# Performance work log

Measured on AMD Instinct MI355X. Metric: run time of the kernel, lower is better.

The kernel has to match this reference:

```python
import jax, jax.numpy as jnp
import numpy as np

IN_C, OUT_C, K, N_FILTERS, STRIDE, PAD = 256, 512, 3, 64, 1, 1


def setup_inputs() -> dict:
    key = jax.random.key(0)
    kx, kw, kb, krw, krb = jax.random.split(key, 5)
    fan_in = IN_C * K * K
    bound = 1.0 / np.sqrt(fan_in)
    x = jax.random.normal(kx, (32, IN_C, 56, 56), dtype=jnp.float32)
    weight = jax.random.uniform(kw, (OUT_C, IN_C, K, K), minval=-bound, maxval=bound, dtype=jnp.float32)
    bias = jax.random.uniform(kb, (OUT_C,), minval=-bound, maxval=bound, dtype=jnp.float32)
    rbound = 1.0 / np.sqrt(IN_C)
    router_w = jax.random.uniform(krw, (OUT_C, IN_C), minval=-rbound, maxval=rbound, dtype=jnp.float32)
    router_b = jax.random.uniform(krb, (OUT_C,), minval=-rbound, maxval=rbound, dtype=jnp.float32)
    return {"x": x, "weight": weight, "bias": bias, "router_w": router_w, "router_b": router_b}


def reference(x, weight, bias, router_w, router_b):
    B = x.shape[0]
    # router: global avg pool -> linear -> top-k channel mask
    pooled = jnp.mean(x, axis=(2, 3))                      # [B, IN_C]
    router_out = pooled @ router_w.T + router_b            # [B, OUT_C]
    _, top_idx = jax.lax.top_k(router_out, N_FILTERS)      # [B, k]
    mask = jnp.zeros((B, OUT_C), dtype=x.dtype).at[jnp.arange(B)[:, None], top_idx].set(1.0)
    # dense conv2d
    conv = jax.lax.conv_general_dilated(
        x, weight, window_strides=(STRIDE, STRIDE), padding=[(PAD, PAD), (PAD, PAD)],
        dimension_numbers=("NCHW", "OIHW", "NCHW"))
    conv = conv + bias[None, :, None, None]
    return conv * mask[:, :, None, None]
```

## Files before the change

### kernel.cpp

```cpp
#include <hip/hip_runtime.h>

#define IN_C   256
#define OUT_C  512
#define WIDTH  56
#define HW     3136
#define KTOT   2304
#define NF     64
#define NU     448
#define NB     32
#define NGRP   8
#define TN     64
#define NTILE  49
#define XROWS  178
#define LDX    40

typedef __bf16 bf16x8 __attribute__((ext_vector_type(8)));
typedef float  f32x4  __attribute__((ext_vector_type(4)));

__global__ __launch_bounds__(256) void pool_kernel(const float* __restrict__ x,
                                                   float* __restrict__ pooled) {
    int bc = blockIdx.x;
    const float4* src = (const float4*)(x + (size_t)bc * HW);
    float s = 0.f;
    for (int i = threadIdx.x; i < HW / 4; i += 256) {
        float4 v = src[i];
        s += v.x + v.y + v.z + v.w;
    }
    #pragma unroll
    for (int off = 32; off > 0; off >>= 1) s += __shfl_down(s, off, 64);
    __shared__ float wsum[4];
    int lane = threadIdx.x & 63, wv = threadIdx.x >> 6;
    if (lane == 0) wsum[wv] = s;
    __syncthreads();
    if (threadIdx.x == 0)
        pooled[bc] = (wsum[0] + wsum[1] + wsum[2] + wsum[3]) * (1.0f / HW);
}

__global__ __launch_bounds__(512) void router_kernel(const float* __restrict__ pooled,
                                                     const float* __restrict__ rw,
                                                     const float* __restrict__ rb,
                                                     int* __restrict__ sel,
                                                     int* __restrict__ unsel) {
    int b = blockIdx.x;
    __shared__ float p[IN_C];
    __shared__ float v[OUT_C];
    __shared__ int   scount, ucount;
    int t = threadIdx.x;
    if (t < IN_C) p[t] = pooled[b * IN_C + t];
    if (t == 0) { scount = 0; ucount = 0; }
    __syncthreads();
    float acc = rb[t];
    const float* wrow = rw + (size_t)t * IN_C;
    for (int i = 0; i < IN_C; ++i) acc += p[i] * wrow[i];
    v[t] = acc;
    __syncthreads();
    int cnt = 0;
    for (int j = 0; j < OUT_C; ++j) {
        float o = v[j];
        cnt += (o > acc) || (o == acc && j < t);
    }
    if (cnt < NF) {
        int pos = atomicAdd(&scount, 1);
        sel[b * NF + pos] = t;
    } else {
        int pos = atomicAdd(&ucount, 1);
        unsel[b * NU + pos] = t;
    }
}

__global__ __launch_bounds__(256) void compact_w(const float* __restrict__ w,
                                                 const int* __restrict__ sel,
                                                 __bf16* __restrict__ Acomp) {
    int id = blockIdx.x;
    int b = id / 72, rem = id - b * 72;
    int g = rem / 9, tap = rem - g * 9;
    int t = threadIdx.x;
    int oc = t >> 2, q = t & 3;
    int s = sel[b * NF + oc];
    const float* wsrc = w + (size_t)s * KTOT + tap;
    bf16x8 o;
    #pragma unroll
    for (int j = 0; j < 8; ++j)
        o[j] = (__bf16)wsrc[(g * 32 + q * 8 + j) * 9];
    *(bf16x8*)&Acomp[((size_t)id * 64 + oc) * 32 + q * 8] = o;
}

__global__ __launch_bounds__(64) void conv_kernel(const float* __restrict__ x,
                                                  const __bf16* __restrict__ Acomp,
                                                  const float* __restrict__ bias,
                                                  const int* __restrict__ sel,
                                                  const int* __restrict__ unsel,
                                                  float* __restrict__ out) {
    int id   = blockIdx.x;
    int xcd  = id & 7, slot = id >> 3;
    int bq   = slot / NTILE;
    int tile = slot - bq * NTILE;
    int b    = xcd * 4 + bq;
    int ptile = tile * TN;

    int lane = threadIdx.x;
    int fm   = lane & 15, fq = lane >> 4;

    __shared__ __bf16 xlds[XROWS * LDX];

    size_t outb = (size_t)b * OUT_C * HW;

    {
        const int* unselb = unsel + b * NU;
        f32x4 z = {0.f, 0.f, 0.f, 0.f};
        for (int u = fq; u < NU; u += 4) {
            int oc = unselb[u];
            __builtin_nontemporal_store(z, (f32x4*)(out + outb + (size_t)oc * HW + ptile) + fm);
        }
    }

    const float*  x_b    = x + (size_t)b * IN_C * HW;
    const __bf16* a_base = Acomp + (size_t)b * (NGRP * 9 * 64 * 32);

    int pp[4], poh[4], pow_[4];
    #pragma unroll
    for (int s = 0; s < 4; ++s) {
        int p = ptile + s * 16 + fm;
        pp[s]   = p;
        poh[s]  = p / WIDTH;
        pow_[s] = p - poh[s] * WIDTH;
    }

    int gp0[3]; bool act[3];
    #pragma unroll
    for (int it = 0; it < 3; ++it) {
        int sp = it * 64 + lane;
        act[it] = sp < XROWS;
        int gp = ptile - 57 + sp;
        gp = gp < 0 ? 0 : (gp > HW - 1 ? HW - 1 : gp);
        gp0[it] = gp;
    }

    f32x4 acc[4][4] = {};

    #pragma unroll 1
    for (int g = 0; g < NGRP; ++g) {
        #pragma unroll
        for (int it = 0; it < 3; ++it) {
            if (!act[it]) continue;
            int sp = it * 64 + lane;
            const float* sx = x_b + (size_t)(g * 32) * HW + gp0[it];
            #pragma unroll
            for (int oct = 0; oct < 4; ++oct) {
                float v[8];
                #pragma unroll
                for (int j = 0; j < 8; ++j) v[j] = sx[(size_t)(oct * 8 + j) * HW];
                bf16x8 o;
                #pragma unroll
                for (int j = 0; j < 8; ++j) o[j] = (__bf16)v[j];
                *(bf16x8*)&xlds[sp * LDX + oct * 8] = o;
            }
        }
        const __bf16* gp_a = a_base + (size_t)g * 9 * 64 * 32;
        #pragma unroll
        for (int t9 = 0; t9 < 9; ++t9) {
            const int r = t9 / 3, c = t9 - 3 * (t9 / 3);
            const int shift = (r - 1) * WIDTH + (c - 1);
            const __bf16* ap = gp_a + (size_t)t9 * 64 * 32;
            bf16x8 af[4];
            #pragma unroll
            for (int mi = 0; mi < 4; ++mi)
                af[mi] = *(const bf16x8*)(ap + (size_t)(mi * 16 + fm) * 32 + fq * 8);
            #pragma unroll
            for (int s = 0; s < 4; ++s) {
                int ohr = poh[s] + r - 1, owc = pow_[s] + c - 1;
                bool ok = ((unsigned)ohr < 56u) && ((unsigned)owc < 56u);
                bf16x8 bfr = *(const bf16x8*)&xlds[(s * 16 + fm + 57 + shift) * LDX + fq * 8];
                bf16x8 zz = {};
                bfr = ok ? bfr : zz;
                #pragma unroll
                for (int mi = 0; mi < 4; ++mi)
                    acc[mi][s] = __builtin_amdgcn_mfma_f32_16x16x32_bf16(af[mi], bfr, acc[mi][s], 0, 0, 0);
            }
        }
    }

    const int* selb = sel + b * NF;
    #pragma unroll
    for (int mi = 0; mi < 4; ++mi) {
        #pragma unroll
        for (int reg = 0; reg < 4; ++reg) {
            int oc = selb[mi * 16 + fq * 4 + reg];
            float bs = bias[oc];
            float* orow = out + outb + (size_t)oc * HW;
            #pragma unroll
            for (int s = 0; s < 4; ++s)
                __builtin_nontemporal_store(acc[mi][s][reg] + bs, &orow[pp[s]]);
        }
    }
}

extern "C" void kernel_launch(void* const* d_in, const int* in_sizes, int n_in,
                              void* d_out, int out_size, void* d_ws, size_t ws_size,
                              hipStream_t stream) {
    (void)in_sizes; (void)n_in; (void)ws_size; (void)out_size;
    const float* x        = (const float*)d_in[0];
    const float* weight   = (const float*)d_in[1];
    const float* bias     = (const float*)d_in[2];
    const float* router_w = (const float*)d_in[3];
    const float* router_b = (const float*)d_in[4];
    float* out = (float*)d_out;

    char* ws = (char*)d_ws;
    float*  pooled = (float*)ws;
    int*    sel    = (int*)(ws + 32768);
    int*    unsel  = (int*)(ws + 40960);
    __bf16* Acomp  = (__bf16*)(ws + 131072);

    pool_kernel<<<NB * IN_C, 256, 0, stream>>>(x, pooled);
    router_kernel<<<NB, OUT_C, 0, stream>>>(pooled, router_w, router_b, sel, unsel);
    compact_w<<<NB * NGRP * 9, 256, 0, stream>>>(weight, sel, Acomp);

    conv_kernel<<<NTILE * NB, 64, 0, stream>>>(x, Acomp, bias, sel, unsel, out);
}
```

Measured before the change: 374.1 us.

## Pre-transpose input to channel-last bf16 and double-buffer conv tiles via async LDS loads

Adds a transpose kernel that converts x to a pixel-major bf16 layout and computes per-tile pooling partial sums at the same time, so the separate pool kernel is gone. The full weight tensor is reordered into a fragment layout once, with no per-batch gather. The conv kernel now uses 4 waves per block and stages x tiles with global_load_lds into a double-buffered, swizzled LDS layout so the next load overlaps the MFMAs. The cost is an extra bf16 copy of x written and read through memory, and A fragments now come straight from global memory indexed by the selected channels.

```diff
diff --git a/kernel.cpp b/kernel.cpp
--- a/kernel.cpp
+++ b/kernel.cpp
@@ -11,32 +11,70 @@
 #define NGRP   8
 #define TN     64
 #define NTILE  49
-#define XROWS  178
-#define LDX    40
+#define SROWS  192
 
 typedef __bf16 bf16x8 __attribute__((ext_vector_type(8)));
 typedef float  f32x4  __attribute__((ext_vector_type(4)));
 
-__global__ __launch_bounds__(256) void pool_kernel(const float* __restrict__ x,
-                                                   float* __restrict__ pooled) {
-    int bc = blockIdx.x;
-    const float4* src = (const float4*)(x + (size_t)bc * HW);
-    float s = 0.f;
-    for (int i = threadIdx.x; i < HW / 4; i += 256) {
-        float4 v = src[i];
-        s += v.x + v.y + v.z + v.w;
-    }
-    #pragma unroll
-    for (int off = 32; off > 0; off >>= 1) s += __shfl_down(s, off, 64);
-    __shared__ float wsum[4];
-    int lane = threadIdx.x & 63, wv = threadIdx.x >> 6;
-    if (lane == 0) wsum[wv] = s;
-    __syncthreads();
-    if (threadIdx.x == 0)
-        pooled[bc] = (wsum[0] + wsum[1] + wsum[2] + wsum[3]) * (1.0f / HW);
-}
-
-__global__ __launch_bounds__(512) void router_kernel(const float* __restrict__ pooled,
+__global__ __launch_bounds__(256) void xpose_kernel(const float* __restrict__ x,
+                                                    __bf16* __restrict__ xT,
+                                                    float* __restrict__ partial) {
+    int id = blockIdx.x;
+    int b = id / NTILE, tile = id - b * NTILE;
+    int ptile = tile * TN;
+    int tid = threadIdx.x;
+    __shared__ float tl[64][65];
+    __shared__ float plsum[IN_C];
+    const float* xb  = x + (size_t)b * IN_C * HW + ptile;
+    __bf16*      xtb = xT + ((size_t)b * HW + ptile) * IN_C;
+    int pxq  = tid & 15;
+    int rowi = tid >> 4;
+    int px   = tid >> 2;
+    int icq  = tid & 3;
+    for (int chunk = 0; chunk < 4; ++chunk) {
+        #pragma unroll
+        for (int r = 0; r < 4; ++r) {
+            int icL = r * 16 + rowi;
+            int ic  = chunk * 64 + icL;
+            float4 v = *(const float4*)(xb + (size_t)ic * HW + pxq * 4);
+            *(float4*)&tl[icL][pxq * 4] = v;
+            float s = v.x + v.y + v.z + v.w;
+            s += __shfl_down(s, 8, 16);
+            s += __shfl_down(s, 4, 16);
+            s += __shfl_down(s, 2, 16);
+            s += __shfl_down(s, 1, 16);
+            if (pxq == 0) plsum[ic] = s;
+        }
+        __syncthreads();
+        bf16x8 o0, o1;
+        #pragma unroll
+        for (int k = 0; k < 8; ++k) o0[k] = (__bf16)tl[icq * 16 + k][px];
+        #pragma unroll
+        for (int k = 0; k < 8; ++k) o1[k] = (__bf16)tl[icq * 16 + 8 + k][px];
+        __bf16* dst = xtb + (size_t)px * IN_C + chunk * 64 + icq * 16;
+        *(bf16x8*)dst = o0;
+        *(bf16x8*)(dst + 8) = o1;
+        __syncthreads();
+    }
+    partial[(size_t)id * IN_C + tid] = plsum[tid];
+}
+
+__global__ __launch_bounds__(256) void wfrag_kernel(const float* __restrict__ w,
+                                                    __bf16* __restrict__ wf) {
+    int oc = blockIdx.x;
+    const float* src = w + (size_t)oc * KTOT;
+    __bf16* dst = wf + (size_t)oc * KTOT;
+    int tid = threadIdx.x;
+    #pragma unroll
+    for (int rr = 0; rr < 9; ++rr) {
+        int i = rr * 256 + tid;
+        float v = src[i];
+        int ic = i / 9, tap = i - ic * 9;
+        dst[((ic >> 5) * 9 + tap) * 32 + (ic & 31)] = (__bf16)v;
+    }
+}
+
+__global__ __launch_bounds__(512) void router_kernel(const float* __restrict__ partial,
                                                      const float* __restrict__ rw,
                                                      const float* __restrict__ rb,
                                                      int* __restrict__ sel,
@@ -46,7 +84,12 @@
     __shared__ float v[OUT_C];
     __shared__ int   scount, ucount;
     int t = threadIdx.x;
-    if (t < IN_C) p[t] = pooled[b * IN_C + t];
+    if (t < IN_C) {
+        float s = 0.f;
+        const float* pb = partial + (size_t)b * NTILE * IN_C + t;
+        for (int k = 0; k < NTILE; ++k) s += pb[k * IN_C];
+        p[t] = s * (1.0f / HW);
+    }
     if (t == 0) { scount = 0; ucount = 0; }
     __syncthreads();
     float acc = rb[t];
@@ -68,29 +111,12 @@
     }
 }
 
-__global__ __launch_bounds__(256) void compact_w(const float* __restrict__ w,
-                                                 const int* __restrict__ sel,
-                                                 __bf16* __restrict__ Acomp) {
-    int id = blockIdx.x;
-    int b = id / 72, rem = id - b * 72;
-    int g = rem / 9, tap = rem - g * 9;
-    int t = threadIdx.x;
-    int oc = t >> 2, q = t & 3;
-    int s = sel[b * NF + oc];
-    const float* wsrc = w + (size_t)s * KTOT + tap;
-    bf16x8 o;
-    #pragma unroll
-    for (int j = 0; j < 8; ++j)
-        o[j] = (__bf16)wsrc[(g * 32 + q * 8 + j) * 9];
-    *(bf16x8*)&Acomp[((size_t)id * 64 + oc) * 32 + q * 8] = o;
-}
-
-__global__ __launch_bounds__(64) void conv_kernel(const float* __restrict__ x,
-                                                  const __bf16* __restrict__ Acomp,
-                                                  const float* __restrict__ bias,
-                                                  const int* __restrict__ sel,
-                                                  const int* __restrict__ unsel,
-                                                  float* __restrict__ out) {
+__global__ __launch_bounds__(256, 4) void conv_kernel(const __bf16* __restrict__ xT,
+                                                      const __bf16* __restrict__ wf,
+                                                      const float* __restrict__ bias,
+                                                      const int* __restrict__ sel,
+                                                      const int* __restrict__ unsel,
+                                                      float* __restrict__ out) {
     int id   = blockIdx.x;
     int xcd  = id & 7, slot = id >> 3;
     int bq   = slot / NTILE;
@@ -98,101 +124,108 @@
     int b    = xcd * 4 + bq;
     int ptile = tile * TN;
 
-    int lane = threadIdx.x;
+    int tid  = threadIdx.x;
+    int lane = tid & 63, w = tid >> 6;
     int fm   = lane & 15, fq = lane >> 4;
-
-    __shared__ __bf16 xlds[XROWS * LDX];
+    int mi2  = w >> 1,  s2 = w & 1;
+
+    __shared__ __bf16 xlds[2][SROWS * 32];
+    __shared__ int    selLds[NF];
+    __shared__ int    unsLds[NU];
 
     size_t outb = (size_t)b * OUT_C * HW;
+    const __bf16* xtb = xT + (size_t)b * HW * IN_C;
+
+    if (tid < NF) selLds[tid] = sel[b * NF + tid];
+    for (int u = tid; u < NU; u += 256) unsLds[u] = unsel[b * NU + u];
+
+    const __bf16* sga[3];
+    #pragma unroll
+    for (int rnd = 0; rnd < 3; ++rnd) {
+        int row = rnd * 64 + w * 16 + (lane >> 2);
+        int cc  = (lane & 3) ^ ((row >> 1) & 3);
+        int gp  = ptile - 57 + row;
+        gp = gp < 0 ? 0 : (gp > HW - 1 ? HW - 1 : gp);
+        sga[rnd] = xtb + (size_t)gp * IN_C + cc * 8;
+    }
+
+#define STAGE(buf, g) { \
+    _Pragma("unroll") \
+    for (int rnd = 0; rnd < 3; ++rnd) \
+        __builtin_amdgcn_global_load_lds( \
+            (const __attribute__((address_space(1))) void*)(sga[rnd] + (g) * 32), \
+            (__attribute__((address_space(3))) void*)&xlds[buf][(rnd * 64 + w * 16) * 32], \
+            16, 0, 0); }
+
+    int pp[2], poh[2], pow_[2];
+    #pragma unroll
+    for (int sl = 0; sl < 2; ++sl) {
+        int p = ptile + (s2 * 2 + sl) * 16 + fm;
+        pp[sl]   = p;
+        poh[sl]  = p / WIDTH;
+        pow_[sl] = p - poh[sl] * WIDTH;
+    }
+
+    f32x4 acc[2][2] = {};
+
+    STAGE(0, 0);
+    __syncthreads();
 
     {
-        const int* unselb = unsel + b * NU;
         f32x4 z = {0.f, 0.f, 0.f, 0.f};
-        for (int u = fq; u < NU; u += 4) {
-            int oc = unselb[u];
-            __builtin_nontemporal_store(z, (f32x4*)(out + outb + (size_t)oc * HW + ptile) + fm);
-        }
-    }
-
-    const float*  x_b    = x + (size_t)b * IN_C * HW;
-    const __bf16* a_base = Acomp + (size_t)b * (NGRP * 9 * 64 * 32);
-
-    int pp[4], poh[4], pow_[4];
-    #pragma unroll
-    for (int s = 0; s < 4; ++s) {
-        int p = ptile + s * 16 + fm;
-        pp[s]   = p;
-        poh[s]  = p / WIDTH;
-        pow_[s] = p - poh[s] * WIDTH;
-    }
-
-    int gp0[3]; bool act[3];
-    #pragma unroll
-    for (int it = 0; it < 3; ++it) {
-        int sp = it * 64 + lane;
-        act[it] = sp < XROWS;
-        int gp = ptile - 57 + sp;
-        gp = gp < 0 ? 0 : (gp > HW - 1 ? HW - 1 : gp);
-        gp0[it] = gp;
-    }
-
-    f32x4 acc[4][4] = {};
+        int lq = tid & 15;
+        for (int u = tid >> 4; u < NU; u += 16) {
+            int oc = unsLds[u];
+            __builtin_nontemporal_store(z, (f32x4*)(out + outb + (size_t)oc * HW + ptile) + lq);
+        }
+    }
+
+    const __bf16* pA[2];
+    #pragma unroll
+    for (int m = 0; m < 2; ++m)
+        pA[m] = wf + (size_t)selLds[(mi2 * 2 + m) * 16 + fm] * KTOT;
 
     #pragma unroll 1
     for (int g = 0; g < NGRP; ++g) {
-        #pragma unroll
-        for (int it = 0; it < 3; ++it) {
-            if (!act[it]) continue;
-            int sp = it * 64 + lane;
-            const float* sx = x_b + (size_t)(g * 32) * HW + gp0[it];
+        int cur = g & 1;
+        if (g < NGRP - 1) STAGE(cur ^ 1, g + 1);
+        const int gof = g * 9 * 32;
+        #pragma unroll
+        for (int t9 = 0; t9 < 9; ++t9) {
+            const int r = t9 / 3, c = t9 - 3 * r;
+            const int shift = (r - 1) * WIDTH + (c - 1);
+            bf16x8 af0 = *(const bf16x8*)(pA[0] + gof + t9 * 32 + fq * 8);
+            bf16x8 af1 = *(const bf16x8*)(pA[1] + gof + t9 * 32 + fq * 8);
             #pragma unroll
-            for (int oct = 0; oct < 4; ++oct) {
-                float v[8];
-                #pragma unroll
-                for (int j = 0; j < 8; ++j) v[j] = sx[(size_t)(oct * 8 + j) * HW];
-                bf16x8 o;
-                #pragma unroll
-                for (int j = 0; j < 8; ++j) o[j] = (__bf16)v[j];
-                *(bf16x8*)&xlds[sp * LDX + oct * 8] = o;
-            }
-        }
-        const __bf16* gp_a = a_base + (size_t)g * 9 * 64 * 32;
-        #pragma unroll
-        for (int t9 = 0; t9 < 9; ++t9) {
-            const int r = t9 / 3, c = t9 - 3 * (t9 / 3);
-            const int shift = (r - 1) * WIDTH + (c - 1);
-            const __bf16* ap = gp_a + (size_t)t9 * 64 * 32;
-            bf16x8 af[4];
-            #pragma unroll
-            for (int mi = 0; mi < 4; ++mi)
-                af[mi] = *(const bf16x8*)(ap + (size_t)(mi * 16 + fm) * 32 + fq * 8);
-            #pragma unroll
-            for (int s = 0; s < 4; ++s) {
-                int ohr = poh[s] + r - 1, owc = pow_[s] + c - 1;
+            for (int sl = 0; sl < 2; ++sl) {
+                int row = (s2 * 2 + sl) * 16 + fm + 57 + shift;
+                int ohr = poh[sl] + r - 1, owc = pow_[sl] + c - 1;
                 bool ok = ((unsigned)ohr < 56u) && ((unsigned)owc < 56u);
-                bf16x8 bfr = *(const bf16x8*)&xlds[(s * 16 + fm + 57 + shift) * LDX + fq * 8];
+                int sw = fq ^ ((row >> 1) & 3);
+                bf16x8 bfr = *(const bf16x8*)&xlds[cur][row * 32 + sw * 8];
                 bf16x8 zz = {};
                 bfr = ok ? bfr : zz;
-                #pragma unroll
-                for (int mi = 0; mi < 4; ++mi)
-                    acc[mi][s] = __builtin_amdgcn_mfma_f32_16x16x32_bf16(af[mi], bfr, acc[mi][s], 0, 0, 0);
+                acc[0][sl] = __builtin_amdgcn_mfma_f32_16x16x32_bf16(af0, bfr, acc[0][sl], 0, 0, 0);
+                acc[1][sl] = __builtin_amdgcn_mfma_f32_16x16x32_bf16(af1, bfr, acc[1][sl], 0, 0, 0);
             }
         }
-    }
-
-    const int* selb = sel + b * NF;
-    #pragma unroll
-    for (int mi = 0; mi < 4; ++mi) {
+        __syncthreads();
+    }
+
+    #pragma unroll
+    for (int m = 0; m < 2; ++m) {
+        int mi = mi2 * 2 + m;
         #pragma unroll
         for (int reg = 0; reg < 4; ++reg) {
-            int oc = selb[mi * 16 + fq * 4 + reg];
+            int oc = selLds[mi * 16 + fq * 4 + reg];
             float bs = bias[oc];
             float* orow = out + outb + (size_t)oc * HW;
             #pragma unroll
-            for (int s = 0; s < 4; ++s)
-                __builtin_nontemporal_store(acc[mi][s][reg] + bs, &orow[pp[s]]);
-        }
-    }
+            for (int sl = 0; sl < 2; ++sl)
+                __builtin_nontemporal_store(acc[m][sl][reg] + bs, &orow[pp[sl]]);
+        }
+    }
+#undef STAGE
 }
 
 extern "C" void kernel_launch(void* const* d_in, const int* in_sizes, int n_in,
@@ -207,14 +240,14 @@
     float* out = (float*)d_out;
 
     char* ws = (char*)d_ws;
-    float*  pooled = (float*)ws;
-    int*    sel    = (int*)(ws + 32768);
-    int*    unsel  = (int*)(ws + 40960);
-    __bf16* Acomp  = (__bf16*)(ws + 131072);
-
-    pool_kernel<<<NB * IN_C, 256, 0, stream>>>(x, pooled);
-    router_kernel<<<NB, OUT_C, 0, stream>>>(pooled, router_w, router_b, sel, unsel);
-    compact_w<<<NB * NGRP * 9, 256, 0, stream>>>(weight, sel, Acomp);
-
-    conv_kernel<<<NTILE * NB, 64, 0, stream>>>(x, Acomp, bias, sel, unsel, out);
-}
+    float*  partial = (float*)ws;
+    int*    sel     = (int*)(ws + 0x200000);
+    int*    unsel   = (int*)(ws + 0x202000);
+    __bf16* wfb     = (__bf16*)(ws + 0x220000);
+    __bf16* xT      = (__bf16*)(ws + 0x480000);
+
+    xpose_kernel <<<NB * NTILE, 256, 0, stream>>>(x, xT, partial);
+    wfrag_kernel <<<OUT_C,      256, 0, stream>>>(weight, wfb);
+    router_kernel<<<NB,         512, 0, stream>>>(partial, router_w, router_b, sel, unsel);
+    conv_kernel  <<<NTILE * NB, 256, 0, stream>>>(xT, wfb, bias, sel, unsel, out);
+}
```

Result: slower. 440.0 us (+17.6%).
